# Kernel tuning notes

Hardware: AMD Instinct MI355X
Metric: run time of the kernel (lower is better)

## Reference

```python
import jax, jax.numpy as jnp
import numpy as np

D = 256; H = 8; FF = 1024; Q = 128; C = 512; B = 4
HD = D // H

def _ln(x, g, b):
    m = x.mean(-1, keepdims=True)
    v = ((x - m) ** 2).mean(-1, keepdims=True)
    return (x - m) / jnp.sqrt(v + 1e-5) * g + b

def _mha(q, k, v, in_w, in_b, out_w, out_b):
    # q,k,v: (L,B,D) / (S,B,D); in_w: (3D,D) packed q|k|v as in torch MHA
    qp = q @ in_w[:D].T + in_b[:D]
    kp = k @ in_w[D:2*D].T + in_b[D:2*D]
    vp = v @ in_w[2*D:].T + in_b[2*D:]
    L, Bb, _ = qp.shape; S = kp.shape[0]
    qh = qp.reshape(L, Bb, H, HD)
    kh = kp.reshape(S, Bb, H, HD)
    vh = vp.reshape(S, Bb, H, HD)
    scores = jnp.einsum('lbhd,sbhd->bhls', qh, kh) / np.sqrt(HD).astype(np.float32)
    a = jax.nn.softmax(scores, axis=-1)
    o = jnp.einsum('bhls,sbhd->lbhd', a, vh).reshape(L, Bb, D)
    return o @ out_w.T + out_b

def setup_inputs() -> dict:
    key = jax.random.key(0)
    ks = jax.random.split(key, 30)
    def p(k, shape, s=0.02):
        return jax.random.normal(k, shape, jnp.float32) * s
    return {
        'tgt': jax.random.normal(ks[0], (Q, B, D), jnp.float32),
        'memory': jax.random.normal(ks[1], (C, B, D), jnp.float32),
        'query_pos': jax.random.normal(ks[2], (Q, B, D), jnp.float32),
        'relative_pos': jax.random.normal(ks[3], (Q, C, B, D), jnp.float32),
        'ln1_g': jnp.ones((D,), jnp.float32), 'ln1_b': jnp.zeros((D,), jnp.float32),
        'ln2_g': jnp.ones((D,), jnp.float32), 'ln2_b': jnp.zeros((D,), jnp.float32),
        'ln3_g': jnp.ones((D,), jnp.float32), 'ln3_b': jnp.zeros((D,), jnp.float32),
        'in_proj_w': p(ks[4], (3 * D, D)), 'in_proj_b': jnp.zeros((3 * D,), jnp.float32),
        'attn_out_w': p(ks[5], (D, D)), 'attn_out_b': jnp.zeros((D,), jnp.float32),
        'mlp1_w': p(ks[6], (D, D)), 'mlp1_b': jnp.zeros((D,), jnp.float32),
        'mlp2_w': p(ks[7], (D, D)), 'mlp2_b': jnp.zeros((D,), jnp.float32),
        'v_w': p(ks[8], (D, D)), 'v_b': jnp.zeros((D,), jnp.float32),
        'o_w': p(ks[9], (D, D)), 'o_b': jnp.zeros((D,), jnp.float32),
        'ff1_w': p(ks[10], (FF, D)), 'ff1_b': jnp.zeros((FF,), jnp.float32),
        'ff2_w': p(ks[11], (D, FF)), 'ff2_b': jnp.zeros((D,), jnp.float32),
    }

def reference(tgt, memory, query_pos, relative_pos,
              ln1_g, ln1_b, ln2_g, ln2_b, ln3_g, ln3_b,
              in_proj_w, in_proj_b, attn_out_w, attn_out_b,
              mlp1_w, mlp1_b, mlp2_w, mlp2_b,
              v_w, v_b, o_w, o_b, ff1_w, ff1_b, ff2_w, ff2_b):
    # pre-norm self-attention (dropout = identity in eval)
    tgt2 = _ln(tgt, ln1_g, ln1_b)
    qk = tgt2 + query_pos
    sa = _mha(qk, qk, tgt2, in_proj_w, in_proj_b, attn_out_w, attn_out_b)
    tgt = tgt + sa
    # relation-attention branch
    tgt2 = _ln(tgt, ln2_g, ln2_b)                       # (Q,B,D)
    x = tgt2[:, None, :, :] - memory[None, :, :, :] + relative_pos  # (Q,C,B,D)
    h = jax.nn.relu(x @ mlp1_w.T + mlp1_b)
    sim = h @ mlp2_w.T + mlp2_b                          # (Q,C,B,D)
    attn = jax.nn.softmax(sim / np.sqrt(D).astype(np.float32), axis=1)
    v2 = (memory[None, :, :, :] + relative_pos) @ v_w.T + v_b
    t = jnp.einsum('qcbf,qcbf->qbf', attn, v2)           # (Q,B,D)
    t = jax.nn.relu(t @ o_w.T + o_b)
    tgt = t + tgt2
    # FFN
    tgt2 = _ln(tgt, ln3_g, ln3_b)
    ff = jax.nn.relu(tgt2 @ ff1_w.T + ff1_b) @ ff2_w.T + ff2_b
    return tgt + ff
```

## Files before the change

kernel.cpp:

```cpp
#include <hip/hip_runtime.h>
#include <hip/hip_bf16.h>
#include <cstdint>
#include <cstddef>

#define DEV __device__ __forceinline__

typedef __attribute__((ext_vector_type(8))) short short8;
typedef __attribute__((ext_vector_type(4))) float f32x4;

constexpr int Dm  = 256;
constexpr int Qn  = 128;
constexpr int Cn  = 512;
constexpr int Bn  = 4;

DEV unsigned short f2bf(float f){
  unsigned int u = __builtin_bit_cast(unsigned int, f);
  u += 0x7fffu + ((u >> 16) & 1u);
  return (unsigned short)(u >> 16);
}
DEV float bfl(unsigned int u){ return __builtin_bit_cast(float, u << 16); }
DEV float bfh(unsigned int u){ return __builtin_bit_cast(float, u & 0xffff0000u); }
DEV unsigned int pk2(float a, float b){
  return (unsigned int)f2bf(a) | ((unsigned int)f2bf(b) << 16);
}

DEV f32x4 mfma16(short8 a, short8 b, f32x4 c){
  return __builtin_amdgcn_mfma_f32_16x16x32_bf16(a, b, c, 0, 0, 0);
}

DEV short8 ldfrag(const unsigned short* buf, int rowbytes, int row0, int ks, int l){
  int r = row0 + (l & 15);
  int byte = (ks * 64 + ((l >> 4) * 16)) ^ ((r & 7) << 4);
  return *(const short8*)((const char*)buf + r * rowbytes + byte);
}

DEV void gload_lds16(const void* g, void* lds){
  __builtin_amdgcn_global_load_lds(
      (const __attribute__((address_space(1))) unsigned int*)g,
      (__attribute__((address_space(3))) unsigned int*)lds, 16, 0, 0);
}

DEV void packw(unsigned short* dst, const float* src, int j){
  int f = j >> 8, d = j & 255;
  int d8 = d >> 3, e = d & 7;
  int byte = (d8 * 16) ^ ((f & 15) << 4);
  dst[f * 256 + (byte >> 1) + e] = f2bf(src[j]);
}

__global__ __launch_bounds__(256) void conv_all_kernel(
    const float* inw, unsigned short* inw_bf,
    const float* aow, unsigned short* aow_bf,
    const float* ow,  unsigned short* ow_bf,
    const float* f1w, unsigned short* f1w_bf,
    const float* f2w, unsigned short* f2w_bf,
    const float* m1w, unsigned short* w1pk,
    const float* m2w, unsigned short* w2pk,
    const float* vw,  unsigned short* wvpk)
{
  const int total = 196608 + 65536 + 65536 + 262144 + 262144 + 3 * 65536;
  for (int i = blockIdx.x * 256 + threadIdx.x; i < total; i += gridDim.x * 256){
    int j = i;
    if (j < 196608){ inw_bf[j] = f2bf(inw[j]); continue; } j -= 196608;
    if (j < 65536) { aow_bf[j] = f2bf(aow[j]); continue; } j -= 65536;
    if (j < 65536) { ow_bf[j]  = f2bf(ow[j]);  continue; } j -= 65536;
    if (j < 262144){ f1w_bf[j] = f2bf(f1w[j]); continue; } j -= 262144;
    if (j < 262144){ f2w_bf[j] = f2bf(f2w[j]); continue; } j -= 262144;
    if (j < 65536) { packw(w1pk, m1w, j); continue; } j -= 65536;
    if (j < 65536) { packw(w2pk, m2w, j); continue; } j -= 65536;
    packw(wvpk, vw, j);
  }
}

__global__ __launch_bounds__(256) void ln_kernel(
    const float* __restrict__ in, const float* __restrict__ g, const float* __restrict__ bt,
    const float* __restrict__ addp,
    float* __restrict__ outF, unsigned short* __restrict__ outA, unsigned short* __restrict__ outB)
{
  const int r = blockIdx.x, t = threadIdx.x;
  float x = in[(size_t)r * 256 + t];
  float s = x, s2 = x * x;
  #pragma unroll
  for (int m = 1; m < 64; m <<= 1){ s += __shfl_xor(s, m, 64); s2 += __shfl_xor(s2, m, 64); }
  __shared__ float ls[8];
  int w = t >> 6, l = t & 63;
  if (l == 0){ ls[w] = s; ls[4 + w] = s2; }
  __syncthreads();
  s  = ls[0] + ls[1] + ls[2] + ls[3];
  s2 = ls[4] + ls[5] + ls[6] + ls[7];
  float mean = s * (1.f / 256.f);
  float var  = s2 * (1.f / 256.f) - mean * mean;
  float y = (x - mean) * rsqrtf(var + 1e-5f) * g[t] + bt[t];
  size_t o = (size_t)r * 256 + t;
  if (outF) outF[o] = y;
  if (outA) outA[o] = f2bf(y);
  if (outB) outB[o] = f2bf(y + addp[o]);
}

__global__ __launch_bounds__(256, 4) void gemm_kernel(
    const unsigned short* __restrict__ A, const unsigned short* __restrict__ W,
    const float* __restrict__ bias, const float* __restrict__ resid,
    float* __restrict__ Cf, unsigned short* __restrict__ Cb,
    int M, int N, int K, float alpha, int relu)
{
  __shared__ unsigned short As[64 * 64];
  __shared__ unsigned short Ws[64 * 64];
  const int tid = threadIdx.x;
  const int l = tid & 63;
  const int w = tid >> 6;
  const int wm = w >> 1, wn = w & 1;
  const int bm = blockIdx.x * 64, bn = blockIdx.y * 64;
  f32x4 acc[2][2] = {{{0,0,0,0},{0,0,0,0}},{{0,0,0,0},{0,0,0,0}}};

  for (int kc = 0; kc < K; kc += 64){
    __syncthreads();
    #pragma unroll
    for (int i = 0; i < 2; ++i){
      int idx = tid + i * 256;
      int r = idx >> 3, s = idx & 7;
      int byte = (s * 16) ^ ((r & 7) << 4);
      *(short8*)((char*)As + r * 128 + byte) = *(const short8*)(A + (size_t)(bm + r) * K + kc + s * 8);
      *(short8*)((char*)Ws + r * 128 + byte) = *(const short8*)(W + (size_t)(bn + r) * K + kc + s * 8);
    }
    __syncthreads();
    #pragma unroll
    for (int ks = 0; ks < 2; ++ks){
      short8 af[2], bf[2];
      af[0] = ldfrag(As, 128, wm * 32,      ks, l);
      af[1] = ldfrag(As, 128, wm * 32 + 16, ks, l);
      bf[0] = ldfrag(Ws, 128, wn * 32,      ks, l);
      bf[1] = ldfrag(Ws, 128, wn * 32 + 16, ks, l);
      #pragma unroll
      for (int i = 0; i < 2; ++i)
        #pragma unroll
        for (int j = 0; j < 2; ++j)
          acc[i][j] = mfma16(af[i], bf[j], acc[i][j]);
    }
  }
  #pragma unroll
  for (int i = 0; i < 2; ++i)
  #pragma unroll
  for (int j = 0; j < 2; ++j){
    int col = bn + wn * 32 + j * 16 + (l & 15);
    float bv = bias ? bias[col] : 0.f;
    #pragma unroll
    for (int u = 0; u < 4; ++u){
      int row = bm + wm * 32 + i * 16 + ((l >> 4) << 2) + u;
      float v = alpha * acc[i][j][u] + bv;
      if (relu) v = fmaxf(v, 0.f);
      if (resid) v += resid[(size_t)row * N + col];
      if (Cf) Cf[(size_t)row * N + col] = v;
      if (Cb) Cb[(size_t)row * N + col] = f2bf(v);
    }
  }
}

__global__ __launch_bounds__(256) void attn_kernel(
    const float* __restrict__ qkp, const float* __restrict__ vp,
    unsigned short* __restrict__ attn_o)
{
  __shared__ float ks[128][33];
  __shared__ float vs[128][33];
  __shared__ float sc[128][129];
  const int bh = blockIdx.x;
  const int b = bh >> 3, h = bh & 7;
  const int tid = threadIdx.x;
  const int lrow = tid >> 1;
  const int half = tid & 1;
  {
    int s = tid >> 1;
    int d0 = half * 16;
    const float* kp = qkp + ((size_t)s * Bn + b) * 512 + 256 + h * 32 + d0;
    const float* vv = vp  + ((size_t)s * Bn + b) * 256 +       h * 32 + d0;
    #pragma unroll
    for (int d = 0; d < 16; d += 4){
      *(float4*)&ks[s][d0 + d] = *(const float4*)(kp + d);
      *(float4*)&vs[s][d0 + d] = *(const float4*)(vv + d);
    }
  }
  __syncthreads();
  float qv[32];
  const float* qp = qkp + ((size_t)lrow * Bn + b) * 512 + h * 32;
  #pragma unroll
  for (int d = 0; d < 32; ++d) qv[d] = qp[d];
  const float scale = 0.17677669529663687f;
  float mloc = -1e30f;
  for (int s2 = 0; s2 < 64; ++s2){
    int s = half * 64 + s2;
    float dot = 0.f;
    #pragma unroll
    for (int d = 0; d < 32; ++d) dot += qv[d] * ks[s][d];
    dot *= scale;
    sc[lrow][s] = dot;
    mloc = fmaxf(mloc, dot);
  }
  float m = fmaxf(mloc, __shfl_xor(mloc, 1, 64));
  float sum = 0.f;
  for (int s2 = 0; s2 < 64; ++s2){
    int s = half * 64 + s2;
    float e = __expf(sc[lrow][s] - m);
    sum += e;
    sc[lrow][s] = e;
  }
  sum += __shfl_xor(sum, 1, 64);
  float inv = 1.f / sum;
  float o[32];
  #pragma unroll
  for (int d = 0; d < 32; ++d) o[d] = 0.f;
  for (int s2 = 0; s2 < 64; ++s2){
    int s = half * 64 + s2;
    float e = sc[lrow][s];
    #pragma unroll
    for (int d = 0; d < 32; ++d) o[d] += e * vs[s][d];
  }
  #pragma unroll
  for (int d = 0; d < 32; ++d){
    o[d] += __shfl_xor(o[d], 1, 64);
    o[d] *= inv;
  }
  unsigned short* op = attn_o + ((size_t)lrow * Bn + b) * 256 + h * 32 + half * 16;
  #pragma unroll
  for (int d = 0; d < 16; ++d) op[d] = f2bf(o[half * 16 + d]);
}

template<int MODE>
__global__ __launch_bounds__(1024, 4) void relpass_kernel(
    const float* __restrict__ rel, const float* __restrict__ memp,
    const float* __restrict__ t22f,
    const unsigned short* src, const unsigned short* __restrict__ Wg,
    const float* __restrict__ bias, unsigned short* dst,
    unsigned short* ydst, const unsigned short* __restrict__ simsrc)
{
  __shared__ unsigned short Wt[65536];
  __shared__ unsigned short xb[8192];
  const int qb = blockIdx.x;
  const int q = qb >> 2, b = qb & 3;
  const int tid = threadIdx.x;
  const int w = tid >> 6, l = tid & 63;
  const int ch2 = w >> 3, fb = w & 7;
  const int l15 = l & 15, lg = l >> 4;

  #pragma unroll
  for (int i = 0; i < 8; ++i){
    int base = w * 64 + i * 1024;
    gload_lds16((const char*)Wg + ((size_t)base + l) * 16, (char*)Wt + (size_t)base * 16);
  }

  const int row = tid >> 5, d8 = tid & 31;
  const int toff = row * 512 + ((d8 * 16) ^ ((row & 15) << 4));
  const char* srcp = (const char*)src + (size_t)qb * 262144;

  float4 t20, t21;
  float4 r0, r1, m0, m1;
  uint4 stg;
  if constexpr (MODE == 0){
    t20 = *(const float4*)(t22f + (size_t)qb * 256 + d8 * 8);
    t21 = *(const float4*)(t22f + (size_t)qb * 256 + d8 * 8 + 4);
    const float* rp = rel + (((size_t)q * 512 + row) * 4 + b) * 256 + d8 * 8;
    const float* mp = memp + ((size_t)(row * 4 + b)) * 256 + d8 * 8;
    r0 = *(const float4*)rp;  r1 = *(const float4*)(rp + 4);
    m0 = *(const float4*)mp;  m1 = *(const float4*)(mp + 4);
  } else {
    stg = *(const uint4*)(srcp + toff);
  }
  asm volatile("s_waitcnt vmcnt(0)" ::: "memory");
  if constexpr (MODE == 0){
    uint4 xw, yw;
    xw.x = pk2(t20.x - m0.x + r0.x, t20.y - m0.y + r0.y);
    xw.y = pk2(t20.z - m0.z + r0.z, t20.w - m0.w + r0.w);
    xw.z = pk2(t21.x - m1.x + r1.x, t21.y - m1.y + r1.y);
    xw.w = pk2(t21.z - m1.z + r1.z, t21.w - m1.w + r1.w);
    yw.x = pk2(r0.x + m0.x, r0.y + m0.y);
    yw.y = pk2(r0.z + m0.z, r0.w + m0.w);
    yw.z = pk2(r1.x + m1.x, r1.y + m1.y);
    yw.w = pk2(r1.z + m1.z, r1.w + m1.w);
    *(uint4*)((char*)ydst + (size_t)qb * 262144 + toff) = yw;
    *(uint4*)((char*)xb + toff) = xw;
  } else {
    *(uint4*)((char*)xb + toff) = stg;
  }
  __syncthreads();

  float bv[2][4];
  #pragma unroll
  for (int j = 0; j < 2; ++j)
    #pragma unroll
    for (int u = 0; u < 4; ++u)
      bv[j][u] = bias[fb * 32 + j * 16 + lg * 4 + u];

  float ta[2][4], la[2][4];
  if constexpr (MODE == 2){
    #pragma unroll
    for (int j = 0; j < 2; ++j)
      #pragma unroll
      for (int u = 0; u < 4; ++u){ ta[j][u] = 0.f; la[j][u] = 0.f; }
  }

  const int r = ch2 * 16 + l15;
  for (int t = 0; t < 16; ++t){
    if (t < 15){
      if constexpr (MODE == 0){
        int c = (t + 1) * 32 + row;
        const float* rp = rel + (((size_t)q * 512 + c) * 4 + b) * 256 + d8 * 8;
        const float* mp = memp + ((size_t)(c * 4 + b)) * 256 + d8 * 8;
        r0 = *(const float4*)rp;  r1 = *(const float4*)(rp + 4);
        m0 = *(const float4*)mp;  m1 = *(const float4*)(mp + 4);
      } else {
        stg = *(const uint4*)(srcp + (size_t)(t + 1) * 16384 + toff);
      }
    }
    uint4 simv;
    if constexpr (MODE == 2)
      simv = *(const uint4*)((const char*)simsrc + (size_t)qb * 262144 + (size_t)t * 16384 + (size_t)(w * 64 + l) * 16);

    f32x4 acc[2] = {{0,0,0,0},{0,0,0,0}};
    #pragma unroll
    for (int kc = 0; kc < 8; ++kc){
      short8 bx = *(const short8*)((const char*)xb + r * 512 + ((kc * 64 + lg * 16) ^ ((r & 15) << 4)));
      #pragma unroll
      for (int j = 0; j < 2; ++j){
        int f = fb * 32 + j * 16 + l15;
        short8 aw = *(const short8*)((const char*)Wt + f * 512 + ((kc * 64 + lg * 16) ^ ((f & 15) << 4)));
        acc[j] = mfma16(aw, bx, acc[j]);
      }
    }

    if constexpr (MODE == 0){
      int c = t * 32 + r;
      size_t rowb = (size_t)qb * 262144 + (size_t)c * 512;
      #pragma unroll
      for (int j = 0; j < 2; ++j){
        uint2 pk;
        pk.x = pk2(fmaxf(acc[j][0] + bv[j][0], 0.f), fmaxf(acc[j][1] + bv[j][1], 0.f));
        pk.y = pk2(fmaxf(acc[j][2] + bv[j][2], 0.f), fmaxf(acc[j][3] + bv[j][3], 0.f));
        int inrow = (fb * 64 + j * 32 + lg * 8) ^ ((c & 15) << 4);
        *(uint2*)((char*)dst + rowb + inrow) = pk;
      }
    } else if constexpr (MODE == 1){
      uint4 d;
      d.x = pk2((acc[0][0] + bv[0][0]) * 0.0625f, (acc[0][1] + bv[0][1]) * 0.0625f);
      d.y = pk2((acc[0][2] + bv[0][2]) * 0.0625f, (acc[0][3] + bv[0][3]) * 0.0625f);
      d.z = pk2((acc[1][0] + bv[1][0]) * 0.0625f, (acc[1][1] + bv[1][1]) * 0.0625f);
      d.w = pk2((acc[1][2] + bv[1][2]) * 0.0625f, (acc[1][3] + bv[1][3]) * 0.0625f);
      *(uint4*)((char*)dst + (size_t)qb * 262144 + (size_t)t * 16384 + (size_t)(w * 64 + l) * 16) = d;
    } else {
      const unsigned int sv[4] = {simv.x, simv.y, simv.z, simv.w};
      #pragma unroll
      for (int j = 0; j < 2; ++j)
        #pragma unroll
        for (int p = 0; p < 2; ++p){
          unsigned int s2 = sv[j * 2 + p];
          float e0 = __expf(bfl(s2)), e1 = __expf(bfh(s2));
          float v0 = acc[j][p * 2 + 0] + bv[j][p * 2 + 0];
          float v1 = acc[j][p * 2 + 1] + bv[j][p * 2 + 1];
          ta[j][p * 2 + 0] += e0 * v0;  la[j][p * 2 + 0] += e0;
          ta[j][p * 2 + 1] += e1 * v1;  la[j][p * 2 + 1] += e1;
        }
    }

    if (t < 15){
      __syncthreads();
      if constexpr (MODE == 0){
        uint4 xw, yw;
        xw.x = pk2(t20.x - m0.x + r0.x, t20.y - m0.y + r0.y);
        xw.y = pk2(t20.z - m0.z + r0.z, t20.w - m0.w + r0.w);
        xw.z = pk2(t21.x - m1.x + r1.x, t21.y - m1.y + r1.y);
        xw.w = pk2(t21.z - m1.z + r1.z, t21.w - m1.w + r1.w);
        yw.x = pk2(r0.x + m0.x, r0.y + m0.y);
        yw.y = pk2(r0.z + m0.z, r0.w + m0.w);
        yw.z = pk2(r1.x + m1.x, r1.y + m1.y);
        yw.w = pk2(r1.z + m1.z, r1.w + m1.w);
        *(uint4*)((char*)ydst + (size_t)qb * 262144 + (size_t)(t + 1) * 16384 + toff) = yw;
        *(uint4*)((char*)xb + toff) = xw;
      } else {
        *(uint4*)((char*)xb + toff) = stg;
      }
      __syncthreads();
    }
  }

  if constexpr (MODE == 2){
    #pragma unroll
    for (int j = 0; j < 2; ++j)
      #pragma unroll
      for (int u = 0; u < 4; ++u){
        #pragma unroll
        for (int m = 1; m <= 8; m <<= 1){
          ta[j][u] += __shfl_xor(ta[j][u], m, 64);
          la[j][u] += __shfl_xor(la[j][u], m, 64);
        }
      }
    __syncthreads();
    float* bufT = (float*)xb;
    float* bufL = bufT + 512;
    if (l15 == 0){
      #pragma unroll
      for (int j = 0; j < 2; ++j)
        #pragma unroll
        for (int u = 0; u < 4; ++u){
          int f = fb * 32 + j * 16 + lg * 4 + u;
          bufT[ch2 * 256 + f] = ta[j][u];
          bufL[ch2 * 256 + f] = la[j][u];
        }
    }
    __syncthreads();
    if (tid < 256){
      float T = bufT[tid] + bufT[256 + tid];
      float L = bufL[tid] + bufL[256 + tid];
      dst[(size_t)qb * 256 + tid] = f2bf(T / L);
    }
  }
}

extern "C" void kernel_launch(void* const* d_in, const int* in_sizes, int n_in,
                              void* d_out, int out_size, void* d_ws, size_t ws_size,
                              hipStream_t stream)
{
  const float* tgt  = (const float*)d_in[0];
  const float* mem  = (const float*)d_in[1];
  const float* qpos = (const float*)d_in[2];
  const float* rel  = (const float*)d_in[3];
  const float* ln1g = (const float*)d_in[4];
  const float* ln1b = (const float*)d_in[5];
  const float* ln2g = (const float*)d_in[6];
  const float* ln2b = (const float*)d_in[7];
  const float* ln3g = (const float*)d_in[8];
  const float* ln3b = (const float*)d_in[9];
  const float* inw  = (const float*)d_in[10];
  const float* inb  = (const float*)d_in[11];
  const float* aow  = (const float*)d_in[12];
  const float* aob  = (const float*)d_in[13];
  const float* m1w  = (const float*)d_in[14];
  const float* m1b  = (const float*)d_in[15];
  const float* m2w  = (const float*)d_in[16];
  const float* m2b  = (const float*)d_in[17];
  const float* vw   = (const float*)d_in[18];
  const float* vb   = (const float*)d_in[19];
  const float* ow   = (const float*)d_in[20];
  const float* ob   = (const float*)d_in[21];
  const float* f1w  = (const float*)d_in[22];
  const float* f1b  = (const float*)d_in[23];
  const float* f2w  = (const float*)d_in[24];
  const float* f2b  = (const float*)d_in[25];

  char* ws = (char*)d_ws;
  size_t off = 0;
  auto alloc = [&](size_t bytes) -> char* {
    char* p = ws + off; off += (bytes + 255) & ~size_t(255); return p;
  };
  unsigned short* y_sw    = (unsigned short*)alloc((size_t)512 * 512 * 256 * 2);
  unsigned short* h_sw    = (unsigned short*)alloc((size_t)512 * 512 * 256 * 2);
  unsigned short* w1pk    = (unsigned short*)alloc(256 * 256 * 2);
  unsigned short* w2pk    = (unsigned short*)alloc(256 * 256 * 2);
  unsigned short* wvpk    = (unsigned short*)alloc(256 * 256 * 2);
  unsigned short* inw_bf  = (unsigned short*)alloc(768 * 256 * 2);
  unsigned short* aow_bf  = (unsigned short*)alloc(256 * 256 * 2);
  unsigned short* ow_bf   = (unsigned short*)alloc(256 * 256 * 2);
  unsigned short* f1w_bf  = (unsigned short*)alloc(1024 * 256 * 2);
  unsigned short* f2w_bf  = (unsigned short*)alloc(256 * 1024 * 2);
  unsigned short* t21_bf  = (unsigned short*)alloc(512 * 256 * 2);
  unsigned short* qk_bf   = (unsigned short*)alloc(512 * 256 * 2);
  float*          qkp     = (float*)alloc(512 * 512 * 4);
  float*          vp      = (float*)alloc(512 * 256 * 4);
  unsigned short* ao_bf   = (unsigned short*)alloc(512 * 256 * 2);
  float*          tgta    = (float*)alloc(512 * 256 * 4);
  float*          t22_f   = (float*)alloc(512 * 256 * 4);
  unsigned short* trel_bf = (unsigned short*)alloc(512 * 256 * 2);
  float*          tgtr    = (float*)alloc(512 * 256 * 4);
  unsigned short* t23_bf  = (unsigned short*)alloc(512 * 256 * 2);
  unsigned short* ffh_bf  = (unsigned short*)alloc(512 * 1024 * 2);

  conv_all_kernel<<<2048, 256, 0, stream>>>(inw, inw_bf, aow, aow_bf, ow, ow_bf,
      f1w, f1w_bf, f2w, f2w_bf, m1w, w1pk, m2w, w2pk, vw, wvpk);

  ln_kernel<<<512, 256, 0, stream>>>(tgt, ln1g, ln1b, qpos, nullptr, t21_bf, qk_bf);

  gemm_kernel<<<dim3(8, 8), 256, 0, stream>>>(qk_bf, inw_bf, inb, nullptr,
      qkp, nullptr, 512, 512, 256, 1.f, 0);
  gemm_kernel<<<dim3(8, 4), 256, 0, stream>>>(t21_bf, inw_bf + 512 * 256, inb + 512, nullptr,
      vp, nullptr, 512, 256, 256, 1.f, 0);

  attn_kernel<<<32, 256, 0, stream>>>(qkp, vp, ao_bf);

  gemm_kernel<<<dim3(8, 4), 256, 0, stream>>>(ao_bf, aow_bf, aob, tgt,
      tgta, nullptr, 512, 256, 256, 1.f, 0);

  ln_kernel<<<512, 256, 0, stream>>>(tgta, ln2g, ln2b, nullptr, t22_f, nullptr, nullptr);

  relpass_kernel<0><<<512, 1024, 0, stream>>>(rel, mem, t22_f, nullptr, w1pk, m1b,
      h_sw, y_sw, nullptr);
  relpass_kernel<1><<<512, 1024, 0, stream>>>(nullptr, nullptr, nullptr, h_sw, w2pk, m2b,
      h_sw, nullptr, nullptr);
  relpass_kernel<2><<<512, 1024, 0, stream>>>(nullptr, nullptr, nullptr, y_sw, wvpk, vb,
      trel_bf, nullptr, h_sw);

  gemm_kernel<<<dim3(8, 4), 256, 0, stream>>>(trel_bf, ow_bf, ob, t22_f,
      tgtr, nullptr, 512, 256, 256, 1.f, 1);

  ln_kernel<<<512, 256, 0, stream>>>(tgtr, ln3g, ln3b, nullptr, nullptr, t23_bf, nullptr);

  gemm_kernel<<<dim3(8, 16), 256, 0, stream>>>(t23_bf, f1w_bf, f1b, nullptr,
      nullptr, ffh_bf, 512, 1024, 256, 1.f, 1);
  gemm_kernel<<<dim3(8, 4), 256, 0, stream>>>(ffh_bf, f2w_bf, f2b, tgtr,
      (float*)d_out, nullptr, 512, 256, 1024, 1.f, 0);
}
```

Baseline: 373.3 us.

## Fuse three relation-attention passes into one kernel keeping h and y on-chip

Replaces the three relpass kernel launches, which wrote and re-read 128 MB bf16 intermediates (h and y), with one fused kernel that computes x/y per 16-row chunk, runs the MLP1 GEMM from LDS weights, then MLP2 and V projections with weights held in registers, and accumulates the softmax-weighted sum online. This removes large global-memory round trips of the intermediate tensors. In exchange, blocks shrink to 512 threads with 16-row chunks and heavy register use (two 2x8 short8 weight arrays per thread), which may reduce occupancy and MFMA efficiency. The softmax also drops max subtraction, matching the previous kernels.

```diff
diff --git a/kernel.cpp b/kernel.cpp
--- a/kernel.cpp
+++ b/kernel.cpp
@@ -18,8 +18,6 @@
   u += 0x7fffu + ((u >> 16) & 1u);
   return (unsigned short)(u >> 16);
 }
-DEV float bfl(unsigned int u){ return __builtin_bit_cast(float, u << 16); }
-DEV float bfh(unsigned int u){ return __builtin_bit_cast(float, u & 0xffff0000u); }
 DEV unsigned int pk2(float a, float b){
   return (unsigned int)f2bf(a) | ((unsigned int)f2bf(b) << 16);
 }
@@ -222,48 +220,73 @@
   for (int d = 0; d < 16; ++d) op[d] = f2bf(o[half * 16 + d]);
 }
 
-template<int MODE>
-__global__ __launch_bounds__(1024, 4) void relpass_kernel(
+__global__ __launch_bounds__(512, 2) void relfused_kernel(
     const float* __restrict__ rel, const float* __restrict__ memp,
     const float* __restrict__ t22f,
-    const unsigned short* src, const unsigned short* __restrict__ Wg,
-    const float* __restrict__ bias, unsigned short* dst,
-    unsigned short* ydst, const unsigned short* __restrict__ simsrc)
-{
-  __shared__ unsigned short Wt[65536];
-  __shared__ unsigned short xb[8192];
+    const unsigned short* __restrict__ W1g,
+    const unsigned short* __restrict__ W2g,
+    const unsigned short* __restrict__ Wvg,
+    const float* __restrict__ b1, const float* __restrict__ b2,
+    const float* __restrict__ vbp,
+    unsigned short* __restrict__ trel)
+{
+  __shared__ unsigned short W1t[65536];
+  __shared__ unsigned short xb[4096];
+  __shared__ unsigned short yb[4096];
+  __shared__ unsigned short hb[4096];
+
   const int qb = blockIdx.x;
   const int q = qb >> 2, b = qb & 3;
   const int tid = threadIdx.x;
   const int w = tid >> 6, l = tid & 63;
-  const int ch2 = w >> 3, fb = w & 7;
   const int l15 = l & 15, lg = l >> 4;
 
   #pragma unroll
-  for (int i = 0; i < 8; ++i){
-    int base = w * 64 + i * 1024;
-    gload_lds16((const char*)Wg + ((size_t)base + l) * 16, (char*)Wt + (size_t)base * 16);
-  }
-
-  const int row = tid >> 5, d8 = tid & 31;
-  const int toff = row * 512 + ((d8 * 16) ^ ((row & 15) << 4));
-  const char* srcp = (const char*)src + (size_t)qb * 262144;
-
-  float4 t20, t21;
-  float4 r0, r1, m0, m1;
-  uint4 stg;
-  if constexpr (MODE == 0){
-    t20 = *(const float4*)(t22f + (size_t)qb * 256 + d8 * 8);
-    t21 = *(const float4*)(t22f + (size_t)qb * 256 + d8 * 8 + 4);
-    const float* rp = rel + (((size_t)q * 512 + row) * 4 + b) * 256 + d8 * 8;
-    const float* mp = memp + ((size_t)(row * 4 + b)) * 256 + d8 * 8;
-    r0 = *(const float4*)rp;  r1 = *(const float4*)(rp + 4);
-    m0 = *(const float4*)mp;  m1 = *(const float4*)(mp + 4);
-  } else {
-    stg = *(const uint4*)(srcp + toff);
-  }
-  asm volatile("s_waitcnt vmcnt(0)" ::: "memory");
-  if constexpr (MODE == 0){
+  for (int i = 0; i < 16; ++i){
+    int base = (w * 16 + i) * 64;
+    gload_lds16((const char*)W1g + ((size_t)base + l) * 16, (char*)W1t + (size_t)base * 16);
+  }
+
+  short8 w2r[2][8], wvr[2][8];
+  #pragma unroll
+  for (int j = 0; j < 2; ++j){
+    int f = w * 32 + j * 16 + l15;
+    #pragma unroll
+    for (int kc = 0; kc < 8; ++kc){
+      int byte = f * 512 + ((kc * 64 + lg * 16) ^ ((f & 15) << 4));
+      w2r[j][kc] = *(const short8*)((const char*)W2g + byte);
+      wvr[j][kc] = *(const short8*)((const char*)Wvg + byte);
+    }
+  }
+
+  float bv1[2][4], bv2[2][4], bvv[2][4];
+  #pragma unroll
+  for (int j = 0; j < 2; ++j)
+    #pragma unroll
+    for (int u = 0; u < 4; ++u){
+      int f = w * 32 + j * 16 + lg * 4 + u;
+      bv1[j][u] = b1[f]; bv2[j][u] = b2[f]; bvv[j][u] = vbp[f];
+    }
+
+  const int srow = tid >> 5, d8 = tid & 31;
+  const int toff = srow * 512 + ((d8 * 16) ^ ((srow & 15) << 4));
+  const float4 t20 = *(const float4*)(t22f + (size_t)qb * 256 + d8 * 8);
+  const float4 t21 = *(const float4*)(t22f + (size_t)qb * 256 + d8 * 8 + 4);
+  const float* relbase = rel + (((size_t)q * 512 + srow) * 4 + b) * 256 + d8 * 8;
+  const float* membase = memp + ((size_t)(srow * 4 + b)) * 256 + d8 * 8;
+
+  float4 r0 = *(const float4*)relbase;
+  float4 r1 = *(const float4*)(relbase + 4);
+  float4 m0 = *(const float4*)membase;
+  float4 m1 = *(const float4*)(membase + 4);
+
+  float ta[2][4], la[2][4];
+  #pragma unroll
+  for (int j = 0; j < 2; ++j)
+    #pragma unroll
+    for (int u = 0; u < 4; ++u){ ta[j][u] = 0.f; la[j][u] = 0.f; }
+
+  for (int t = 0; t < 32; ++t){
     uint4 xw, yw;
     xw.x = pk2(t20.x - m0.x + r0.x, t20.y - m0.y + r0.y);
     xw.y = pk2(t20.z - m0.z + r0.z, t20.w - m0.w + r0.w);
@@ -273,140 +296,80 @@
     yw.y = pk2(r0.z + m0.z, r0.w + m0.w);
     yw.z = pk2(r1.x + m1.x, r1.y + m1.y);
     yw.w = pk2(r1.z + m1.z, r1.w + m1.w);
-    *(uint4*)((char*)ydst + (size_t)qb * 262144 + toff) = yw;
     *(uint4*)((char*)xb + toff) = xw;
-  } else {
-    *(uint4*)((char*)xb + toff) = stg;
-  }
-  __syncthreads();
-
-  float bv[2][4];
-  #pragma unroll
-  for (int j = 0; j < 2; ++j)
-    #pragma unroll
-    for (int u = 0; u < 4; ++u)
-      bv[j][u] = bias[fb * 32 + j * 16 + lg * 4 + u];
-
-  float ta[2][4], la[2][4];
-  if constexpr (MODE == 2){
-    #pragma unroll
-    for (int j = 0; j < 2; ++j)
-      #pragma unroll
-      for (int u = 0; u < 4; ++u){ ta[j][u] = 0.f; la[j][u] = 0.f; }
-  }
-
-  const int r = ch2 * 16 + l15;
-  for (int t = 0; t < 16; ++t){
-    if (t < 15){
-      if constexpr (MODE == 0){
-        int c = (t + 1) * 32 + row;
-        const float* rp = rel + (((size_t)q * 512 + c) * 4 + b) * 256 + d8 * 8;
-        const float* mp = memp + ((size_t)(c * 4 + b)) * 256 + d8 * 8;
-        r0 = *(const float4*)rp;  r1 = *(const float4*)(rp + 4);
-        m0 = *(const float4*)mp;  m1 = *(const float4*)(mp + 4);
-      } else {
-        stg = *(const uint4*)(srcp + (size_t)(t + 1) * 16384 + toff);
-      }
-    }
-    uint4 simv;
-    if constexpr (MODE == 2)
-      simv = *(const uint4*)((const char*)simsrc + (size_t)qb * 262144 + (size_t)t * 16384 + (size_t)(w * 64 + l) * 16);
-
-    f32x4 acc[2] = {{0,0,0,0},{0,0,0,0}};
+    *(uint4*)((char*)yb + toff) = yw;
+    if (t < 31){
+      const float* rp = relbase + (size_t)(t + 1) * 16384;
+      const float* mp = membase + (size_t)(t + 1) * 16384;
+      r0 = *(const float4*)rp;  r1 = *(const float4*)(rp + 4);
+      m0 = *(const float4*)mp;  m1 = *(const float4*)(mp + 4);
+    }
+    if (t == 0) asm volatile("s_waitcnt vmcnt(0)" ::: "memory");
+    __syncthreads();
+
+    f32x4 acch[2] = {{0,0,0,0},{0,0,0,0}};
     #pragma unroll
     for (int kc = 0; kc < 8; ++kc){
-      short8 bx = *(const short8*)((const char*)xb + r * 512 + ((kc * 64 + lg * 16) ^ ((r & 15) << 4)));
+      short8 bx = *(const short8*)((const char*)xb + l15 * 512 + ((kc * 64 + lg * 16) ^ (l15 << 4)));
       #pragma unroll
       for (int j = 0; j < 2; ++j){
-        int f = fb * 32 + j * 16 + l15;
-        short8 aw = *(const short8*)((const char*)Wt + f * 512 + ((kc * 64 + lg * 16) ^ ((f & 15) << 4)));
-        acc[j] = mfma16(aw, bx, acc[j]);
+        int f = w * 32 + j * 16 + l15;
+        short8 aw = *(const short8*)((const char*)W1t + f * 512 + ((kc * 64 + lg * 16) ^ ((f & 15) << 4)));
+        acch[j] = mfma16(aw, bx, acch[j]);
       }
     }
-
-    if constexpr (MODE == 0){
-      int c = t * 32 + r;
-      size_t rowb = (size_t)qb * 262144 + (size_t)c * 512;
+    #pragma unroll
+    for (int j = 0; j < 2; ++j){
+      uint2 hp;
+      hp.x = pk2(fmaxf(acch[j][0] + bv1[j][0], 0.f), fmaxf(acch[j][1] + bv1[j][1], 0.f));
+      hp.y = pk2(fmaxf(acch[j][2] + bv1[j][2], 0.f), fmaxf(acch[j][3] + bv1[j][3], 0.f));
+      int inrow = (w * 64 + j * 32 + lg * 8) ^ (l15 << 4);
+      *(uint2*)((char*)hb + l15 * 512 + inrow) = hp;
+    }
+    __syncthreads();
+
+    f32x4 accs[2] = {{0,0,0,0},{0,0,0,0}};
+    f32x4 accv[2] = {{0,0,0,0},{0,0,0,0}};
+    #pragma unroll
+    for (int kc = 0; kc < 8; ++kc){
+      int inb = (kc * 64 + lg * 16) ^ (l15 << 4);
+      short8 bh = *(const short8*)((const char*)hb + l15 * 512 + inb);
+      short8 by = *(const short8*)((const char*)yb + l15 * 512 + inb);
       #pragma unroll
       for (int j = 0; j < 2; ++j){
-        uint2 pk;
-        pk.x = pk2(fmaxf(acc[j][0] + bv[j][0], 0.f), fmaxf(acc[j][1] + bv[j][1], 0.f));
-        pk.y = pk2(fmaxf(acc[j][2] + bv[j][2], 0.f), fmaxf(acc[j][3] + bv[j][3], 0.f));
-        int inrow = (fb * 64 + j * 32 + lg * 8) ^ ((c & 15) << 4);
-        *(uint2*)((char*)dst + rowb + inrow) = pk;
+        accs[j] = mfma16(w2r[j][kc], bh, accs[j]);
+        accv[j] = mfma16(wvr[j][kc], by, accv[j]);
       }
-    } else if constexpr (MODE == 1){
-      uint4 d;
-      d.x = pk2((acc[0][0] + bv[0][0]) * 0.0625f, (acc[0][1] + bv[0][1]) * 0.0625f);
-      d.y = pk2((acc[0][2] + bv[0][2]) * 0.0625f, (acc[0][3] + bv[0][3]) * 0.0625f);
-      d.z = pk2((acc[1][0] + bv[1][0]) * 0.0625f, (acc[1][1] + bv[1][1]) * 0.0625f);
-      d.w = pk2((acc[1][2] + bv[1][2]) * 0.0625f, (acc[1][3] + bv[1][3]) * 0.0625f);
-      *(uint4*)((char*)dst + (size_t)qb * 262144 + (size_t)t * 16384 + (size_t)(w * 64 + l) * 16) = d;
-    } else {
-      const unsigned int sv[4] = {simv.x, simv.y, simv.z, simv.w};
-      #pragma unroll
-      for (int j = 0; j < 2; ++j)
-        #pragma unroll
-        for (int p = 0; p < 2; ++p){
-          unsigned int s2 = sv[j * 2 + p];
-          float e0 = __expf(bfl(s2)), e1 = __expf(bfh(s2));
-          float v0 = acc[j][p * 2 + 0] + bv[j][p * 2 + 0];
-          float v1 = acc[j][p * 2 + 1] + bv[j][p * 2 + 1];
-          ta[j][p * 2 + 0] += e0 * v0;  la[j][p * 2 + 0] += e0;
-          ta[j][p * 2 + 1] += e1 * v1;  la[j][p * 2 + 1] += e1;
-        }
-    }
-
-    if (t < 15){
-      __syncthreads();
-      if constexpr (MODE == 0){
-        uint4 xw, yw;
-        xw.x = pk2(t20.x - m0.x + r0.x, t20.y - m0.y + r0.y);
-        xw.y = pk2(t20.z - m0.z + r0.z, t20.w - m0.w + r0.w);
-        xw.z = pk2(t21.x - m1.x + r1.x, t21.y - m1.y + r1.y);
-        xw.w = pk2(t21.z - m1.z + r1.z, t21.w - m1.w + r1.w);
-        yw.x = pk2(r0.x + m0.x, r0.y + m0.y);
-        yw.y = pk2(r0.z + m0.z, r0.w + m0.w);
-        yw.z = pk2(r1.x + m1.x, r1.y + m1.y);
-        yw.w = pk2(r1.z + m1.z, r1.w + m1.w);
-        *(uint4*)((char*)ydst + (size_t)qb * 262144 + (size_t)(t + 1) * 16384 + toff) = yw;
-        *(uint4*)((char*)xb + toff) = xw;
-      } else {
-        *(uint4*)((char*)xb + toff) = stg;
-      }
-      __syncthreads();
-    }
-  }
-
-  if constexpr (MODE == 2){
+    }
     #pragma unroll
     for (int j = 0; j < 2; ++j)
       #pragma unroll
       for (int u = 0; u < 4; ++u){
-        #pragma unroll
-        for (int m = 1; m <= 8; m <<= 1){
-          ta[j][u] += __shfl_xor(ta[j][u], m, 64);
-          la[j][u] += __shfl_xor(la[j][u], m, 64);
-        }
+        float e = __expf((accs[j][u] + bv2[j][u]) * 0.0625f);
+        float v2 = accv[j][u] + bvv[j][u];
+        ta[j][u] += e * v2;
+        la[j][u] += e;
       }
-    __syncthreads();
-    float* bufT = (float*)xb;
-    float* bufL = bufT + 512;
-    if (l15 == 0){
+    if (t < 31) __syncthreads();
+  }
+
+  #pragma unroll
+  for (int j = 0; j < 2; ++j)
+    #pragma unroll
+    for (int u = 0; u < 4; ++u){
       #pragma unroll
-      for (int j = 0; j < 2; ++j)
-        #pragma unroll
-        for (int u = 0; u < 4; ++u){
-          int f = fb * 32 + j * 16 + lg * 4 + u;
-          bufT[ch2 * 256 + f] = ta[j][u];
-          bufL[ch2 * 256 + f] = la[j][u];
-        }
-    }
-    __syncthreads();
-    if (tid < 256){
-      float T = bufT[tid] + bufT[256 + tid];
-      float L = bufL[tid] + bufL[256 + tid];
-      dst[(size_t)qb * 256 + tid] = f2bf(T / L);
+      for (int m = 1; m <= 8; m <<= 1){
+        ta[j][u] += __shfl_xor(ta[j][u], m, 64);
+        la[j][u] += __shfl_xor(la[j][u], m, 64);
+      }
+    }
+  if (l15 == 0){
+    #pragma unroll
+    for (int j = 0; j < 2; ++j){
+      uint2 o;
+      o.x = pk2(ta[j][0] / la[j][0], ta[j][1] / la[j][1]);
+      o.y = pk2(ta[j][2] / la[j][2], ta[j][3] / la[j][3]);
+      *(uint2*)(trel + (size_t)qb * 256 + w * 32 + j * 16 + lg * 4) = o;
     }
   }
 }
@@ -447,8 +410,6 @@
   auto alloc = [&](size_t bytes) -> char* {
     char* p = ws + off; off += (bytes + 255) & ~size_t(255); return p;
   };
-  unsigned short* y_sw    = (unsigned short*)alloc((size_t)512 * 512 * 256 * 2);
-  unsigned short* h_sw    = (unsigned short*)alloc((size_t)512 * 512 * 256 * 2);
   unsigned short* w1pk    = (unsigned short*)alloc(256 * 256 * 2);
   unsigned short* w2pk    = (unsigned short*)alloc(256 * 256 * 2);
   unsigned short* wvpk    = (unsigned short*)alloc(256 * 256 * 2);
@@ -486,12 +447,8 @@
 
   ln_kernel<<<512, 256, 0, stream>>>(tgta, ln2g, ln2b, nullptr, t22_f, nullptr, nullptr);
 
-  relpass_kernel<0><<<512, 1024, 0, stream>>>(rel, mem, t22_f, nullptr, w1pk, m1b,
-      h_sw, y_sw, nullptr);
-  relpass_kernel<1><<<512, 1024, 0, stream>>>(nullptr, nullptr, nullptr, h_sw, w2pk, m2b,
-      h_sw, nullptr, nullptr);
-  relpass_kernel<2><<<512, 1024, 0, stream>>>(nullptr, nullptr, nullptr, y_sw, wvpk, vb,
-      trel_bf, nullptr, h_sw);
+  relfused_kernel<<<512, 512, 0, stream>>>(rel, mem, t22_f, w1pk, w2pk, wvpk,
+      m1b, m2b, vb, trel_bf);
 
   gemm_kernel<<<dim3(8, 4), 256, 0, stream>>>(trel_bf, ow_bf, ob, t22_f,
       tgtr, nullptr, 512, 256, 256, 1.f, 1);
```

Measured after the change: 331.0 us. 11.3% less time.
